# Kernel tuning notes

Hardware: AMD Instinct MI355X
Metric: run time of the kernel (lower is better)

The kernel has to match this reference:

```python
import jax, jax.numpy as jnp
import numpy as np

ALPHA = 1.0
EPS_CLAMP = 1e-7
EPS_REL = 1e-5


def _pairwise_euc(batch):
    # squared distances via Gram matrix (faithful to torch.norm(b[:,None]-b, dim=2, p=2))
    n2 = jnp.sum(batch * batch, axis=1)                      # [2N]
    sq = n2[:, None] + n2[None, :] - 2.0 * (batch @ batch.T)  # [2N,2N]
    sq = jnp.maximum(sq, 0.0)
    # safe sqrt (torch.norm has zero subgradient at 0)
    safe = jnp.where(sq > 0.0, sq, 1.0)
    return jnp.where(sq > 0.0, jnp.sqrt(safe), 0.0)


def reference(h1, h2, h3):
    n = h1.shape[0]
    batch = jnp.concatenate([h1, h2], axis=0)                # [2N,D]
    dists = _pairwise_euc(batch)
    dists = jnp.maximum(dists, EPS_CLAMP)                    # torch.clamp(min=1e-7)

    # [2N,2N,2N]: d(a,p) - d(a,n)
    differences = dists[:, :, None] - dists[:, None, :]
    triplet = differences + ALPHA

    labels = jnp.concatenate([jnp.arange(n), jnp.arange(n)])
    mask = (labels[None, :] == labels[:, None]).astype(jnp.float32)
    mask = mask - jnp.eye(2 * n, dtype=jnp.float32)          # [2N,2N]
    # torch broadcasting aligns mask with the TRAILING two dims of triplet
    triplet = mask[None, :, :] * triplet
    triplet = jnp.maximum(triplet, 0.0)

    pos = triplet > EPS_REL
    cnt = jnp.sum(pos)
    mean_relevant = jnp.sum(jnp.where(pos, triplet, 0.0)) / cnt.astype(jnp.float32)

    good = jnp.sum(triplet < EPS_REL)
    bad = triplet.size - good

    mean_norm_sq = jnp.mean(jnp.sum(batch * batch, axis=1))
    loss = mean_relevant + 1e-4 * mean_norm_sq
    return (loss, jnp.mean(differences), good, bad, jnp.sqrt(mean_norm_sq))


def setup_inputs() -> dict:
    key = jax.random.key(0)
    k1, k2, k3 = jax.random.split(key, 3)
    N, D = 256, 512
    return {
        "h1": jax.random.normal(k1, (N, D), dtype=jnp.float32),
        "h2": jax.random.normal(k2, (N, D), dtype=jnp.float32),
        "h3": jax.random.normal(k3, (N, D), dtype=jnp.float32),
    }
```

## Files before the change

### kernel.cpp

```cpp
#include <hip/hip_runtime.h>


#define NHALF 256
#define M 512
#define DDIM 512

typedef __attribute__((ext_vector_type(8))) short bf16x8;
typedef __attribute__((ext_vector_type(4))) float f32x4;

__device__ __forceinline__ unsigned short f2bf_rne(float f) {
    unsigned int x = __float_as_uint(f);
    x += 0x7FFFu + ((x >> 16) & 1u);
    return (unsigned short)(x >> 16);
}

__device__ __forceinline__ float distf(float n2a, float n2b, float g) {
    float sq = n2a + n2b - 2.0f * g;
    sq = fmaxf(sq, 0.0f);
    float d = (sq > 0.0f) ? sqrtf(sq) : 0.0f;
    return fmaxf(d, 1e-7f);
}

__global__ __launch_bounds__(256) void prep_kernel(const float* __restrict__ h1,
                                                   const float* __restrict__ h2,
                                                   unsigned short* __restrict__ X,
                                                   float* __restrict__ n2) {
    const int idx = blockIdx.x * 256 + threadIdx.x;
    const float4 v = (idx < 32768) ? ((const float4*)h1)[idx]
                                   : ((const float4*)h2)[idx - 32768];
    ushort4 o;
    o.x = f2bf_rne(v.x); o.y = f2bf_rne(v.y);
    o.z = f2bf_rne(v.z); o.w = f2bf_rne(v.w);
    ((ushort4*)X)[idx] = o;

    float s = v.x * v.x + v.y * v.y + v.z * v.z + v.w * v.w;
#pragma unroll
    for (int off = 32; off > 0; off >>= 1) s += __shfl_down(s, off, 64);

    __shared__ float wsum[4];
    const int lane = threadIdx.x & 63, w = threadIdx.x >> 6;
    if (lane == 0) wsum[w] = s;
    __syncthreads();
    if (threadIdx.x == 0)   n2[blockIdx.x * 2]     = wsum[0] + wsum[1];
    if (threadIdx.x == 128) n2[blockIdx.x * 2 + 1] = wsum[2] + wsum[3];
}

__global__ __launch_bounds__(128) void gram_kernel(const unsigned short* __restrict__ X,
                                                   const float* __restrict__ n2,
                                                   float* __restrict__ psum,
                                                   unsigned int* __restrict__ pcp,
                                                   unsigned int* __restrict__ pcl) {
    const int tid  = threadIdx.x;
    const int wave = tid >> 6, lane = tid & 63;
    const int a0 = blockIdx.y * 32 + wave * 16;
    const int p0 = blockIdx.x * 16;

    const int rsel = lane & 15;
    const int koff = (lane >> 4) * 8;
    const unsigned short* pa = X + (size_t)(a0 + rsel) * DDIM + koff;
    const unsigned short* pb = X + (size_t)(p0 + rsel) * DDIM + koff;
    const unsigned short* pc = X + (size_t)(p0 + NHALF + rsel) * DDIM + koff;

    f32x4 accB = {0.f, 0.f, 0.f, 0.f};
    f32x4 accC = {0.f, 0.f, 0.f, 0.f};
#pragma unroll
    for (int k0 = 0; k0 < DDIM; k0 += 32) {
        bf16x8 av = *(const bf16x8*)(pa + k0);
        bf16x8 bv = *(const bf16x8*)(pb + k0);
        bf16x8 cv = *(const bf16x8*)(pc + k0);
        accB = __builtin_amdgcn_mfma_f32_16x16x32_bf16(av, bv, accB, 0, 0, 0);
        accC = __builtin_amdgcn_mfma_f32_16x16x32_bf16(av, cv, accC, 0, 0, 0);
    }

    const int quad = lane >> 4;
    const int pcol = p0 + (lane & 15);
    const float n2b = n2[pcol];
    const float n2c = n2[pcol + NHALF];
    float lsum = 0.0f;
    unsigned int lcp = 0u, lcl = 0u;
#pragma unroll
    for (int r = 0; r < 4; ++r) {
        const float n2a = n2[a0 + quad * 4 + r];
        const float db = distf(n2a, n2b, accB[r]);
        const float dc = distf(n2a, n2c, accC[r]);
        const float t0 = fmaxf(db - dc + 1.0f, 0.0f);
        const float t1 = fmaxf(dc - db + 1.0f, 0.0f);
        if (t0 > 1e-5f) { lsum += t0; lcp++; }
        if (t0 < 1e-5f) lcl++;
        if (t1 > 1e-5f) { lsum += t1; lcp++; }
        if (t1 < 1e-5f) lcl++;
    }

#pragma unroll
    for (int off = 32; off > 0; off >>= 1) {
        lsum += __shfl_down(lsum, off, 64);
        lcp  += __shfl_down(lcp,  off, 64);
        lcl  += __shfl_down(lcl,  off, 64);
    }
    __shared__ float    s_sum[2];
    __shared__ unsigned s_cp[2], s_cl[2];
    if (lane == 0) { s_sum[wave] = lsum; s_cp[wave] = lcp; s_cl[wave] = lcl; }
    __syncthreads();
    if (tid == 0) {
        const int b = blockIdx.y * gridDim.x + blockIdx.x;
        psum[b] = s_sum[0] + s_sum[1];
        pcp[b]  = s_cp[0] + s_cp[1];
        pcl[b]  = s_cl[0] + s_cl[1];
    }
}

__global__ __launch_bounds__(256) void final_kernel(const float* __restrict__ n2,
                                                    const float* __restrict__ psum,
                                                    const unsigned int* __restrict__ pcp,
                                                    const unsigned int* __restrict__ pcl,
                                                    float* __restrict__ out) {
    const int t = threadIdx.x;
    float s = psum[t];
    unsigned int cp = pcp[t], cl = pcl[t];
    float ns = n2[t] + n2[t + NHALF];
#pragma unroll
    for (int off = 32; off > 0; off >>= 1) {
        s  += __shfl_down(s,  off, 64);
        cp += __shfl_down(cp, off, 64);
        cl += __shfl_down(cl, off, 64);
        ns += __shfl_down(ns, off, 64);
    }
    __shared__ float    w_s[4], w_ns[4];
    __shared__ unsigned w_cp[4], w_cl[4];
    const int lane = t & 63, w = t >> 6;
    if (lane == 0) { w_s[w] = s; w_ns[w] = ns; w_cp[w] = cp; w_cl[w] = cl; }
    __syncthreads();
    if (t == 0) {
        const float sum_pos = w_s[0] + w_s[1] + w_s[2] + w_s[3];
        const float sum_n2  = w_ns[0] + w_ns[1] + w_ns[2] + w_ns[3];
        const unsigned cpt = w_cp[0] + w_cp[1] + w_cp[2] + w_cp[3];
        const unsigned clt = w_cl[0] + w_cl[1] + w_cl[2] + w_cl[3];
        const float mean_norm_sq = sum_n2 / (float)M;
        out[0] = sum_pos / (float)cpt + 1e-4f * mean_norm_sq;
        out[1] = 0.0f;
        out[2] = (float)(133955584u + clt);
        out[3] = (float)(262144u - clt);
        out[4] = sqrtf(mean_norm_sq);
    }
}

extern "C" void kernel_launch(void* const* d_in, const int* in_sizes, int n_in,
                              void* d_out, int out_size, void* d_ws, size_t ws_size,
                              hipStream_t stream) {
    const float* h1 = (const float*)d_in[0];
    const float* h2 = (const float*)d_in[1];
    char* w = (char*)d_ws;
    unsigned short* X  = (unsigned short*)w;
    float* n2          = (float*)(w + 512 * 1024);
    float* psum        = (float*)(w + 512 * 1024 + 2048);
    unsigned int* pcp  = (unsigned int*)(w + 512 * 1024 + 3072);
    unsigned int* pcl  = (unsigned int*)(w + 512 * 1024 + 4096);
    float* out = (float*)d_out;

    prep_kernel<<<256, 256, 0, stream>>>(h1, h2, X, n2);
    gram_kernel<<<dim3(16, 16), 128, 0, stream>>>(X, n2, psum, pcp, pcl);
    final_kernel<<<1, 256, 0, stream>>>(n2, psum, pcp, pcl, out);
}
```

Baseline: 66.06 us.

## Fuse bf16 conversion, Gram MFMA and final reduction into a single kernel

Removes the separate prep and final kernels. The Gram kernel now reads fp32 inputs directly, converts them to bf16 in registers, and computes the row norms on the fly. The final reduction is done by whichever block arrives last, detected with an atomic counter, which is reset each call by a memset. This removes two kernel launches and the bf16 staging buffer, at the cost of doubling per-block global read traffic (fp32 instead of bf16) and redundant conversion across blocks.

Measured after the change: 71.84 us. +8.8%, slower.

```diff
diff --git a/kernel.cpp b/kernel.cpp
--- a/kernel.cpp
+++ b/kernel.cpp
@@ -1,4 +1,5 @@
 #include <hip/hip_runtime.h>
+#include <hip/hip_bf16.h>
 
 
 #define NHALF 256
@@ -8,79 +9,72 @@
 typedef __attribute__((ext_vector_type(8))) short bf16x8;
 typedef __attribute__((ext_vector_type(4))) float f32x4;
 
-__device__ __forceinline__ unsigned short f2bf_rne(float f) {
-    unsigned int x = __float_as_uint(f);
-    x += 0x7FFFu + ((x >> 16) & 1u);
-    return (unsigned short)(x >> 16);
+union BF8 { bf16x8 v; __hip_bfloat162 h[4]; };
+
+__device__ __forceinline__ bf16x8 cvt8(float4 lo, float4 hi) {
+    BF8 u;
+    u.h[0] = __float22bfloat162_rn(make_float2(lo.x, lo.y));
+    u.h[1] = __float22bfloat162_rn(make_float2(lo.z, lo.w));
+    u.h[2] = __float22bfloat162_rn(make_float2(hi.x, hi.y));
+    u.h[3] = __float22bfloat162_rn(make_float2(hi.z, hi.w));
+    return u.v;
+}
+
+__device__ __forceinline__ float sq4(float4 v) {
+    return v.x * v.x + v.y * v.y + v.z * v.z + v.w * v.w;
 }
 
 __device__ __forceinline__ float distf(float n2a, float n2b, float g) {
-    float sq = n2a + n2b - 2.0f * g;
-    sq = fmaxf(sq, 0.0f);
+    float sq = fmaxf(n2a + n2b - 2.0f * g, 0.0f);
     float d = (sq > 0.0f) ? sqrtf(sq) : 0.0f;
     return fmaxf(d, 1e-7f);
 }
 
-__global__ __launch_bounds__(256) void prep_kernel(const float* __restrict__ h1,
-                                                   const float* __restrict__ h2,
-                                                   unsigned short* __restrict__ X,
-                                                   float* __restrict__ n2) {
-    const int idx = blockIdx.x * 256 + threadIdx.x;
-    const float4 v = (idx < 32768) ? ((const float4*)h1)[idx]
-                                   : ((const float4*)h2)[idx - 32768];
-    ushort4 o;
-    o.x = f2bf_rne(v.x); o.y = f2bf_rne(v.y);
-    o.z = f2bf_rne(v.z); o.w = f2bf_rne(v.w);
-    ((ushort4*)X)[idx] = o;
-
-    float s = v.x * v.x + v.y * v.y + v.z * v.z + v.w * v.w;
-#pragma unroll
-    for (int off = 32; off > 0; off >>= 1) s += __shfl_down(s, off, 64);
-
-    __shared__ float wsum[4];
-    const int lane = threadIdx.x & 63, w = threadIdx.x >> 6;
-    if (lane == 0) wsum[w] = s;
-    __syncthreads();
-    if (threadIdx.x == 0)   n2[blockIdx.x * 2]     = wsum[0] + wsum[1];
-    if (threadIdx.x == 128) n2[blockIdx.x * 2 + 1] = wsum[2] + wsum[3];
-}
-
-__global__ __launch_bounds__(128) void gram_kernel(const unsigned short* __restrict__ X,
-                                                   const float* __restrict__ n2,
-                                                   float* __restrict__ psum,
-                                                   unsigned int* __restrict__ pcp,
-                                                   unsigned int* __restrict__ pcl) {
-    const int tid  = threadIdx.x;
-    const int wave = tid >> 6, lane = tid & 63;
+__global__ __launch_bounds__(128) void fused_kernel(const float* __restrict__ h1,
+                                                    const float* __restrict__ h2,
+                                                    float* __restrict__ psum,
+                                                    unsigned int* __restrict__ pcp,
+                                                    unsigned int* __restrict__ pcl,
+                                                    float* __restrict__ nsum,
+                                                    unsigned int* __restrict__ ctr,
+                                                    float* __restrict__ out) {
+    const int tid = threadIdx.x, wave = tid >> 6, lane = tid & 63;
     const int a0 = blockIdx.y * 32 + wave * 16;
     const int p0 = blockIdx.x * 16;
+    const int rsel = lane & 15, koff = (lane >> 4) * 8;
 
-    const int rsel = lane & 15;
-    const int koff = (lane >> 4) * 8;
-    const unsigned short* pa = X + (size_t)(a0 + rsel) * DDIM + koff;
-    const unsigned short* pb = X + (size_t)(p0 + rsel) * DDIM + koff;
-    const unsigned short* pc = X + (size_t)(p0 + NHALF + rsel) * DDIM + koff;
+    const float* pa = ((a0 < NHALF) ? h1 + (size_t)(a0 + rsel) * DDIM
+                                    : h2 + (size_t)(a0 - NHALF + rsel) * DDIM) + koff;
+    const float* pb = h1 + (size_t)(p0 + rsel) * DDIM + koff;
+    const float* pc = h2 + (size_t)(p0 + rsel) * DDIM + koff;
 
     f32x4 accB = {0.f, 0.f, 0.f, 0.f};
     f32x4 accC = {0.f, 0.f, 0.f, 0.f};
+    float nA = 0.f, nB = 0.f, nC = 0.f;
 #pragma unroll
     for (int k0 = 0; k0 < DDIM; k0 += 32) {
-        bf16x8 av = *(const bf16x8*)(pa + k0);
-        bf16x8 bv = *(const bf16x8*)(pb + k0);
-        bf16x8 cv = *(const bf16x8*)(pc + k0);
-        accB = __builtin_amdgcn_mfma_f32_16x16x32_bf16(av, bv, accB, 0, 0, 0);
-        accC = __builtin_amdgcn_mfma_f32_16x16x32_bf16(av, cv, accC, 0, 0, 0);
+        float4 al = *(const float4*)(pa + k0), ah = *(const float4*)(pa + k0 + 4);
+        float4 bl = *(const float4*)(pb + k0), bh = *(const float4*)(pb + k0 + 4);
+        float4 cl = *(const float4*)(pc + k0), ch = *(const float4*)(pc + k0 + 4);
+        nA += sq4(al) + sq4(ah);
+        nB += sq4(bl) + sq4(bh);
+        nC += sq4(cl) + sq4(ch);
+        bf16x8 av = cvt8(al, ah);
+        accB = __builtin_amdgcn_mfma_f32_16x16x32_bf16(av, cvt8(bl, bh), accB, 0, 0, 0);
+        accC = __builtin_amdgcn_mfma_f32_16x16x32_bf16(av, cvt8(cl, ch), accC, 0, 0, 0);
     }
 
+    nA += __shfl_xor(nA, 16, 64); nA += __shfl_xor(nA, 32, 64);
+    nB += __shfl_xor(nB, 16, 64); nB += __shfl_xor(nB, 32, 64);
+    nC += __shfl_xor(nC, 16, 64); nC += __shfl_xor(nC, 32, 64);
+
     const int quad = lane >> 4;
-    const int pcol = p0 + (lane & 15);
-    const float n2b = n2[pcol];
-    const float n2c = n2[pcol + NHALF];
-    float lsum = 0.0f;
+    const float n2b = nB, n2c = nC;
+    float lsum = 0.f;
     unsigned int lcp = 0u, lcl = 0u;
 #pragma unroll
     for (int r = 0; r < 4; ++r) {
-        const float n2a = n2[a0 + quad * 4 + r];
+        const float n2a = __shfl(nA, quad * 4 + r, 64);
         const float db = distf(n2a, n2b, accB[r]);
         const float dc = distf(n2a, n2c, accC[r]);
         const float t0 = fmaxf(db - dc + 1.0f, 0.0f);
@@ -91,56 +85,58 @@
         if (t1 < 1e-5f) lcl++;
     }
 
+    float wnA = nA;
 #pragma unroll
     for (int off = 32; off > 0; off >>= 1) {
         lsum += __shfl_down(lsum, off, 64);
         lcp  += __shfl_down(lcp,  off, 64);
         lcl  += __shfl_down(lcl,  off, 64);
+        wnA  += __shfl_down(wnA,  off, 64);
     }
-    __shared__ float    s_sum[2];
-    __shared__ unsigned s_cp[2], s_cl[2];
-    if (lane == 0) { s_sum[wave] = lsum; s_cp[wave] = lcp; s_cl[wave] = lcl; }
+
+    __shared__ float    s_f[2], s_n[2];
+    __shared__ unsigned s_p[2], s_l[2];
+    __shared__ int      s_last;
+    if (lane == 0) { s_f[wave] = lsum; s_p[wave] = lcp; s_l[wave] = lcl; s_n[wave] = wnA; }
     __syncthreads();
     if (tid == 0) {
-        const int b = blockIdx.y * gridDim.x + blockIdx.x;
-        psum[b] = s_sum[0] + s_sum[1];
-        pcp[b]  = s_cp[0] + s_cp[1];
-        pcl[b]  = s_cl[0] + s_cl[1];
+        const int b = blockIdx.y * 16 + blockIdx.x;
+        atomicExch(&psum[b], s_f[0] + s_f[1]);
+        atomicExch(&pcp[b],  s_p[0] + s_p[1]);
+        atomicExch(&pcl[b],  s_l[0] + s_l[1]);
+        if (blockIdx.x == 0)
+            atomicExch(&nsum[blockIdx.y], (s_n[0] + s_n[1]) * 0.25f);
+        __threadfence();
+        s_last = (atomicAdd(ctr, 1u) == 255u);
     }
-}
+    __syncthreads();
 
-__global__ __launch_bounds__(256) void final_kernel(const float* __restrict__ n2,
-                                                    const float* __restrict__ psum,
-                                                    const unsigned int* __restrict__ pcp,
-                                                    const unsigned int* __restrict__ pcl,
-                                                    float* __restrict__ out) {
-    const int t = threadIdx.x;
-    float s = psum[t];
-    unsigned int cp = pcp[t], cl = pcl[t];
-    float ns = n2[t] + n2[t + NHALF];
+    if (s_last) {
+        __threadfence();
+        float    fs  = atomicAdd(&psum[tid], 0.0f) + atomicAdd(&psum[tid + 128], 0.0f);
+        unsigned cp2 = atomicAdd(&pcp[tid], 0u)    + atomicAdd(&pcp[tid + 128], 0u);
+        unsigned cl2 = atomicAdd(&pcl[tid], 0u)    + atomicAdd(&pcl[tid + 128], 0u);
+        float    ns  = (tid < 16) ? atomicAdd(&nsum[tid], 0.0f) : 0.0f;
 #pragma unroll
-    for (int off = 32; off > 0; off >>= 1) {
-        s  += __shfl_down(s,  off, 64);
-        cp += __shfl_down(cp, off, 64);
-        cl += __shfl_down(cl, off, 64);
-        ns += __shfl_down(ns, off, 64);
-    }
-    __shared__ float    w_s[4], w_ns[4];
-    __shared__ unsigned w_cp[4], w_cl[4];
-    const int lane = t & 63, w = t >> 6;
-    if (lane == 0) { w_s[w] = s; w_ns[w] = ns; w_cp[w] = cp; w_cl[w] = cl; }
-    __syncthreads();
-    if (t == 0) {
-        const float sum_pos = w_s[0] + w_s[1] + w_s[2] + w_s[3];
-        const float sum_n2  = w_ns[0] + w_ns[1] + w_ns[2] + w_ns[3];
-        const unsigned cpt = w_cp[0] + w_cp[1] + w_cp[2] + w_cp[3];
-        const unsigned clt = w_cl[0] + w_cl[1] + w_cl[2] + w_cl[3];
-        const float mean_norm_sq = sum_n2 / (float)M;
-        out[0] = sum_pos / (float)cpt + 1e-4f * mean_norm_sq;
-        out[1] = 0.0f;
-        out[2] = (float)(133955584u + clt);
-        out[3] = (float)(262144u - clt);
-        out[4] = sqrtf(mean_norm_sq);
+        for (int off = 32; off > 0; off >>= 1) {
+            fs  += __shfl_down(fs,  off, 64);
+            cp2 += __shfl_down(cp2, off, 64);
+            cl2 += __shfl_down(cl2, off, 64);
+            ns  += __shfl_down(ns,  off, 64);
+        }
+        if (lane == 0) { s_f[wave] = fs; s_p[wave] = cp2; s_l[wave] = cl2; s_n[wave] = ns; }
+        __syncthreads();
+        if (tid == 0) {
+            const float sum_pos = s_f[0] + s_f[1];
+            const unsigned cpt = s_p[0] + s_p[1];
+            const unsigned clt = s_l[0] + s_l[1];
+            const float mns = (s_n[0] + s_n[1]) / (float)M;
+            out[0] = sum_pos / (float)cpt + 1e-4f * mns;
+            out[1] = 0.0f;
+            out[2] = (float)(133955584u + clt);
+            out[3] = (float)(262144u - clt);
+            out[4] = sqrtf(mns);
+        }
     }
 }
 
@@ -150,14 +146,13 @@
     const float* h1 = (const float*)d_in[0];
     const float* h2 = (const float*)d_in[1];
     char* w = (char*)d_ws;
-    unsigned short* X  = (unsigned short*)w;
-    float* n2          = (float*)(w + 512 * 1024);
-    float* psum        = (float*)(w + 512 * 1024 + 2048);
-    unsigned int* pcp  = (unsigned int*)(w + 512 * 1024 + 3072);
-    unsigned int* pcl  = (unsigned int*)(w + 512 * 1024 + 4096);
+    float* psum       = (float*)(w);
+    unsigned int* pcp = (unsigned int*)(w + 1024);
+    unsigned int* pcl = (unsigned int*)(w + 2048);
+    float* nsum       = (float*)(w + 3072);
+    unsigned int* ctr = (unsigned int*)(w + 4096);
     float* out = (float*)d_out;
 
-    prep_kernel<<<256, 256, 0, stream>>>(h1, h2, X, n2);
-    gram_kernel<<<dim3(16, 16), 128, 0, stream>>>(X, n2, psum, pcp, pcl);
-    final_kernel<<<1, 256, 0, stream>>>(n2, psum, pcp, pcl, out);
+    hipMemsetAsync(ctr, 0, 4, stream);
+    fused_kernel<<<dim3(16, 16), 128, 0, stream>>>(h1, h2, psum, pcp, pcl, nsum, ctr, out);
 }
```
